# Performance work log

Measured on AMD Instinct MI355X. Metric: run time of the kernel, lower is better.

The kernel has to match this reference:

```python
import jax, jax.numpy as jnp
import numpy as np

S = 2048          # input sequence length
H_TOT = 4096      # total history tokens
NHIST = 1024      # number of history segments
LOC, TIM, UID = 50000, 48, 1000
D_LOC, D_TIM, D_UID, HID = 512, 64, 64, 512
D_IN = D_LOC + D_TIM          # 576, GRU input size
TARGET = 1024


def setup_inputs() -> dict:
    key = jax.random.key(0)
    ks = jax.random.split(key, 16)
    n = lambda k, shp, s=0.02: jax.random.normal(k, shp, dtype=jnp.float32) * s
    return {
        "loc": jax.random.randint(ks[0], (S, 1), 0, LOC),
        "tim": jax.random.randint(ks[1], (S, 1), 0, TIM),
        "history_loc": jax.random.randint(ks[2], (H_TOT, 1), 0, LOC),
        "history_tim": jax.random.randint(ks[3], (H_TOT, 1), 0, TIM),
        "history_count": jnp.full((NHIST,), H_TOT // NHIST, dtype=jnp.int32),
        "uid": jax.random.randint(ks[4], (1,), 0, UID),
        "target_len": TARGET,
        "emb_loc": n(ks[5], (LOC, D_LOC)),
        "emb_tim": n(ks[6], (TIM, D_TIM)),
        "emb_uid": n(ks[7], (UID, D_UID)),
        "fc_attn_w": n(ks[8], (HID, D_IN), 0.05),
        "fc_attn_b": jnp.zeros((HID,), jnp.float32),
        "w_ih": n(ks[9], (3 * HID, D_IN), 0.05),
        "w_hh": n(ks[10], (3 * HID, HID), 0.05),
        "b_ih": jnp.zeros((3 * HID,), jnp.float32),
        "b_hh": jnp.zeros((3 * HID,), jnp.float32),
        "fc_final_w": n(ks[11], (LOC, 2 * HID + D_UID), 0.05),
        "fc_final_b": jnp.zeros((LOC,), jnp.float32),
    }


def _gru(x, w_ih, w_hh, b_ih, b_hh):
    # x: [S, D_IN]; batch size 1 -> carry a single hidden vector. PyTorch GRU cell.
    gi = x @ w_ih.T + b_ih  # [S, 3H] (input projections precomputed)

    def step(h, gi_t):
        gh = w_hh @ h + b_hh
        i_r, i_z, i_n = jnp.split(gi_t, 3)
        h_r, h_z, h_n = jnp.split(gh, 3)
        r = jax.nn.sigmoid(i_r + h_r)
        z = jax.nn.sigmoid(i_z + h_z)
        nn_ = jnp.tanh(i_n + r * h_n)
        h_new = (1.0 - z) * nn_ + z * h
        return h_new, h_new

    _, out = jax.lax.scan(step, jnp.zeros((HID,), x.dtype), gi)
    return out  # [S, HID]


def reference(loc, tim, history_loc, history_tim, history_count, uid, target_len,
              emb_loc, emb_tim, emb_uid, fc_attn_w, fc_attn_b,
              w_ih, w_hh, b_ih, b_hh, fc_final_w, fc_final_b):
    # current trajectory embeddings (dropout is identity at eval)
    x = jnp.concatenate([emb_loc[loc[:, 0]], emb_tim[tim[:, 0]]], axis=1)  # [S, D_IN]

    # ragged segment-mean pooling of history loc embeddings, first-token tim embedding
    hist_le = emb_loc[history_loc[:, 0]]  # [H_TOT, D_LOC]
    hist_te = emb_tim[history_tim[:, 0]]  # [H_TOT, D_TIM]
    counts = history_count
    seg_ids = jnp.repeat(jnp.arange(NHIST), counts, total_repeat_length=H_TOT)
    loc2 = jax.ops.segment_sum(hist_le, seg_ids, num_segments=NHIST)
    loc2 = loc2 / counts[:, None].astype(loc2.dtype)
    offsets = jnp.cumsum(counts) - counts  # start index of each segment
    tim2 = hist_te[offsets]
    history = jnp.tanh(jnp.concatenate([loc2, tim2], axis=1) @ fc_attn_w.T + fc_attn_b)  # [NHIST, HID]

    out_state = _gru(x, w_ih, w_hh, b_ih, b_hh)  # [S, HID]
    q = out_state[-target_len:]                  # [T, HID]

    # dot attention: replaces the python double loop with one matmul + softmax
    attn = jax.nn.softmax(q @ history.T, axis=-1)  # [T, NHIST]
    context = attn @ history                       # [T, HID]

    uid_emb = jnp.broadcast_to(emb_uid[uid[0]], (target_len, D_UID))
    out = jnp.concatenate([q, context, uid_emb], axis=1)  # [T, 2H+D_UID]
    y = out @ fc_final_w.T + fc_final_b                   # [T, LOC]
    return jax.nn.log_softmax(y, axis=-1)
```

## Files before the change

### kernel.cpp

```cpp
#include <hip/hip_runtime.h>
#include <cstddef>

typedef unsigned short u16;
typedef unsigned int u32;

#define S_LEN   2048
#define H_TOT   4096
#define NHIST   1024
#define D_LOC   512
#define D_TIM   64
#define D_UID   64
#define HID     512
#define D_IN    576
#define TARGET  1024
#define NLOC    50000
#define D_OUT   1088
#define G3      1536

__device__ __forceinline__ u16 f2bf(float f) {
    u32 x; __builtin_memcpy(&x, &f, 4);
    u32 r = x + 0x7fffu + ((x >> 16) & 1u);
    return (u16)(r >> 16);
}
__device__ __forceinline__ float bf2f(u16 u) {
    u32 x = ((u32)u) << 16;
    float f; __builtin_memcpy(&f, &x, 4); return f;
}
__device__ __forceinline__ float u32_as_f32(u32 x) {
    float f; __builtin_memcpy(&f, &x, 4); return f;
}
__device__ __forceinline__ float sigm(float x) {
    return 1.0f / (1.0f + __expf(-x));
}
__device__ __forceinline__ float tanh_stable(float x) {
    float a = __expf(-2.0f * fabsf(x));
    float t = (1.0f - a) / (1.0f + a);
    return copysignf(t, x);
}
__device__ __forceinline__ u32 pk(float a, float b) {
    return (u32)f2bf(a) | ((u32)f2bf(b) << 16);
}

typedef __bf16 bf16x8 __attribute__((ext_vector_type(8)));
typedef float  f32x4  __attribute__((ext_vector_type(4)));

__global__ __launch_bounds__(1024) void scan_kernel(const int* __restrict__ counts,
                                                    int* __restrict__ offs) {
    __shared__ int s[NHIST];
    int tid = threadIdx.x;
    int v = counts[tid];
    s[tid] = v;
    __syncthreads();
    for (int d = 1; d < NHIST; d <<= 1) {
        int t = (tid >= d) ? s[tid - d] : 0;
        __syncthreads();
        s[tid] += t;
        __syncthreads();
    }
    offs[tid] = s[tid] - v;
}

__global__ __launch_bounds__(64) void hist_kernel(const int* __restrict__ hloc,
                                                  const int* __restrict__ htim,
                                                  const int* __restrict__ counts,
                                                  const int* __restrict__ offs,
                                                  const float* __restrict__ emb_loc,
                                                  const float* __restrict__ emb_tim,
                                                  u16* __restrict__ hist2) {
    int i = blockIdx.x, c = threadIdx.x;
    int off = offs[i], cnt = counts[i];
    float a[8] = {};
    for (int k = 0; k < cnt; k++) {
        int kk = off + k; if (kk >= H_TOT) break;
        const float* p = emb_loc + (size_t)hloc[kk] * D_LOC + c * 8;
        float4 q0 = ((const float4*)p)[0];
        float4 q1 = ((const float4*)p)[1];
        a[0] += q0.x; a[1] += q0.y; a[2] += q0.z; a[3] += q0.w;
        a[4] += q1.x; a[5] += q1.y; a[6] += q1.z; a[7] += q1.w;
    }
    float inv = (cnt > 0) ? 1.0f / (float)cnt : 0.0f;
    u16* o = hist2 + (size_t)i * D_IN + c * 8;
    #pragma unroll
    for (int j = 0; j < 8; j++) o[j] = f2bf(a[j] * inv);
    hist2[(size_t)i * D_IN + D_LOC + c] = f2bf(emb_tim[(size_t)htim[off] * D_TIM + c]);
}

__global__ __launch_bounds__(256) void build_x_kernel(const int* __restrict__ loc,
                                                      const int* __restrict__ tim,
                                                      const float* __restrict__ emb_loc,
                                                      const float* __restrict__ emb_tim,
                                                      u16* __restrict__ x) {
    int idx = blockIdx.x * 256 + threadIdx.x;
    int row = idx / D_IN, col = idx - row * D_IN;
    float v = (col < D_LOC) ? emb_loc[(size_t)loc[row] * D_LOC + col]
                            : emb_tim[(size_t)tim[row] * D_TIM + (col - D_LOC)];
    x[idx] = f2bf(v);
}

__global__ __launch_bounds__(256) void uid_kernel(const int* __restrict__ uid,
                                                  const float* __restrict__ emb_uid,
                                                  u16* __restrict__ outbuf) {
    int idx = blockIdx.x * 256 + threadIdx.x;
    int row = idx >> 6, c = idx & 63;
    outbuf[(size_t)row * D_OUT + 2 * HID + c] = f2bf(emb_uid[(size_t)uid[0] * D_UID + c]);
}

template<int EPI, bool OBF16, bool NG, bool AF32, bool BF32>
__global__ __launch_bounds__(256)
void gemm_bt_kernel(const void* __restrict__ Ap, const void* __restrict__ Bp,
                    void* __restrict__ Cp, const float* __restrict__ bias,
                    u16* __restrict__ Ct,
                    int M, int N, int K, int lda, int ldb, int ldc, int ldt) {
    __shared__ __align__(16) u16 sA[128 * 64];
    __shared__ __align__(16) u16 sB[128 * 64];
    const int tid = threadIdx.x;
    const int w = tid >> 6, lane = tid & 63;
    const int wr = (w >> 1) * 64, wc = (w & 1) * 64;
    const int m0 = blockIdx.y * 128, n0 = blockIdx.x * 128;
    f32x4 acc[4][4] = {};
    const int srow = w * 32 + (lane >> 3);
    const int scol = (lane & 7) * 8;

    for (int kt = 0; kt < K; kt += 64) {
        #pragma unroll
        for (int i = 0; i < 4; i++) {
            int rt = srow + i * 8;
            int ra = m0 + rt;
            if (AF32) {
                const float* s = (const float*)Ap + (size_t)ra * lda + kt + scol;
                float4 x0 = ((const float4*)s)[0];
                float4 x1 = ((const float4*)s)[1];
                uint4 q = { pk(x0.x, x0.y), pk(x0.z, x0.w), pk(x1.x, x1.y), pk(x1.z, x1.w) };
                *(uint4*)&sA[rt * 64 + scol] = q;
            } else {
                *(uint4*)&sA[rt * 64 + scol] =
                    *(const uint4*)((const u16*)Ap + (size_t)ra * lda + kt + scol);
            }
            int rb = n0 + rt;
            if (NG) rb = (rb < N - 1) ? rb : (N - 1);
            if (BF32) {
                const float* s = (const float*)Bp + (size_t)rb * ldb + kt + scol;
                float4 x0 = ((const float4*)s)[0];
                float4 x1 = ((const float4*)s)[1];
                uint4 q = { pk(x0.x, x0.y), pk(x0.z, x0.w), pk(x1.x, x1.y), pk(x1.z, x1.w) };
                *(uint4*)&sB[rt * 64 + scol] = q;
            } else {
                *(uint4*)&sB[rt * 64 + scol] =
                    *(const uint4*)((const u16*)Bp + (size_t)rb * ldb + kt + scol);
            }
        }
        __syncthreads();
        #pragma unroll
        for (int kk = 0; kk < 64; kk += 32) {
            const int krow = kk + (lane >> 4) * 8;
            bf16x8 af[4], bf_[4];
            #pragma unroll
            for (int mi = 0; mi < 4; mi++)
                af[mi] = *(const bf16x8*)&sA[(wr + mi * 16 + (lane & 15)) * 64 + krow];
            #pragma unroll
            for (int ni = 0; ni < 4; ni++)
                bf_[ni] = *(const bf16x8*)&sB[(wc + ni * 16 + (lane & 15)) * 64 + krow];
            #pragma unroll
            for (int mi = 0; mi < 4; mi++)
                #pragma unroll
                for (int ni = 0; ni < 4; ni++)
                    acc[mi][ni] = __builtin_amdgcn_mfma_f32_16x16x32_bf16(
                        af[mi], bf_[ni], acc[mi][ni], 0, 0, 0);
        }
        __syncthreads();
    }
    #pragma unroll
    for (int mi = 0; mi < 4; mi++) {
        #pragma unroll
        for (int ni = 0; ni < 4; ni++) {
            int gc = n0 + wc + ni * 16 + (lane & 15);
            if (NG && gc >= N) continue;
            #pragma unroll
            for (int r = 0; r < 4; r++) {
                int gr = m0 + wr + mi * 16 + (lane >> 4) * 4 + r;
                float v = acc[mi][ni][r];
                if (EPI & 1) v += bias[gc];
                if (EPI & 2) v = tanh_stable(v);
                if (OBF16) ((u16*)Cp)[(size_t)gr * ldc + gc] = f2bf(v);
                else       ((float*)Cp)[(size_t)gr * ldc + gc] = v;
                if (EPI & 4) Ct[(size_t)gc * ldt + gr] = f2bf(v);
            }
        }
    }
}

#define GRU_BLOCKS 16
__global__ __launch_bounds__(384, 2)
void gru_kernel(const float* __restrict__ gi, const float* __restrict__ w_hh,
                const float* __restrict__ b_hh, u32* __restrict__ hcomm,
                u16* __restrict__ outbuf) {
    const int b = blockIdx.x, tid = threadIdx.x;
    const int wr = tid % 96, qd = tid / 96;
    const int g = wr >> 5, jj = wr & 31;
    const int grow = g * HID + b * 32 + jj;

    __shared__ __align__(16) float hbuf[HID];
    __shared__ float psum[96 * 4];
    __shared__ float ghh[96], gii[96];

    float wreg[128];
    {
        const float4* wp = (const float4*)(w_hh + (size_t)grow * HID + qd * 128);
        #pragma unroll
        for (int c = 0; c < 32; c++) {
            float4 v = wp[c];
            wreg[c * 4 + 0] = v.x; wreg[c * 4 + 1] = v.y;
            wreg[c * 4 + 2] = v.z; wreg[c * 4 + 3] = v.w;
        }
    }
    float bhh = b_hh[grow];
    for (int i = tid; i < HID; i += 384) hbuf[i] = 0.0f;
    float gi_cur = (qd == 0) ? gi[grow] : 0.0f;
    __syncthreads();

    for (int t = 0; t < S_LEN; t++) {
        float acc = 0.0f;
        const float4* hp = (const float4*)(hbuf + qd * 128);
        #pragma unroll
        for (int c = 0; c < 32; c++) {
            float4 h4 = hp[c];
            acc = fmaf(wreg[4 * c + 0], h4.x, acc);
            acc = fmaf(wreg[4 * c + 1], h4.y, acc);
            acc = fmaf(wreg[4 * c + 2], h4.z, acc);
            acc = fmaf(wreg[4 * c + 3], h4.w, acc);
        }
        psum[wr * 4 + qd] = acc;
        __syncthreads();
        if (tid < 96) {
            float s = psum[tid * 4] + psum[tid * 4 + 1] + psum[tid * 4 + 2] + psum[tid * 4 + 3];
            ghh[tid] = s + bhh;
            gii[tid] = gi_cur;
        }
        __syncthreads();

        const u32 want = (u32)(t + 1);
        const int p = (t + 1) & 1;
        if (tid < 32) {
            float r = sigm(gii[tid] + ghh[tid]);
            float z = sigm(gii[32 + tid] + ghh[32 + tid]);
            float n = tanh_stable(gii[64 + tid] + r * ghh[64 + tid]);
            float hn = (1.0f - z) * n + z * hbuf[b * 32 + tid];
            u32 bits = (u32)f2bf(hn);
            __hip_atomic_store(&hcomm[p * HID + b * 32 + tid], (bits << 16) | want,
                               __ATOMIC_RELAXED, __HIP_MEMORY_SCOPE_AGENT);
            if (t >= (S_LEN - TARGET))
                outbuf[(size_t)(t - (S_LEN - TARGET)) * D_OUT + b * 32 + tid] = (u16)bits;
        }
        float gi_nxt = 0.0f;
        if (qd == 0) {
            int tn = (t + 1 < S_LEN) ? (t + 1) : (S_LEN - 1);
            gi_nxt = gi[(size_t)tn * G3 + grow];
        }
        if (t < S_LEN - 1) {
            u32 v;
            int w0 = tid;
            do {
                v = __hip_atomic_load(&hcomm[p * HID + w0], __ATOMIC_RELAXED, __HIP_MEMORY_SCOPE_AGENT);
            } while ((v & 0xffffu) != want);
            hbuf[w0] = u32_as_f32(v & 0xffff0000u);
            if (tid < 128) {
                int w1 = 384 + tid;
                do {
                    v = __hip_atomic_load(&hcomm[p * HID + w1], __ATOMIC_RELAXED, __HIP_MEMORY_SCOPE_AGENT);
                } while ((v & 0xffffu) != want);
                hbuf[w1] = u32_as_f32(v & 0xffff0000u);
            }
        }
        __syncthreads();
        gi_cur = gi_nxt;
    }
}

__global__ __launch_bounds__(256) void softmax_kernel(const float* __restrict__ sc,
                                                      u16* __restrict__ attn) {
    int r = blockIdx.x, tid = threadIdx.x;
    int lane = tid & 63, wv = tid >> 6;
    const float* row = sc + (size_t)r * NHIST;
    float v[4], m = -3.4e38f;
    #pragma unroll
    for (int k = 0; k < 4; k++) { v[k] = row[tid + 256 * k]; m = fmaxf(m, v[k]); }
    #pragma unroll
    for (int o = 32; o >= 1; o >>= 1) m = fmaxf(m, __shfl_xor(m, o));
    __shared__ float rmax[4], rsum[4];
    if (lane == 0) rmax[wv] = m;
    __syncthreads();
    m = fmaxf(fmaxf(rmax[0], rmax[1]), fmaxf(rmax[2], rmax[3]));
    float s = 0.0f;
    #pragma unroll
    for (int k = 0; k < 4; k++) { v[k] = __expf(v[k] - m); s += v[k]; }
    #pragma unroll
    for (int o = 32; o >= 1; o >>= 1) s += __shfl_xor(s, o);
    if (lane == 0) rsum[wv] = s;
    __syncthreads();
    s = rsum[0] + rsum[1] + rsum[2] + rsum[3];
    float inv = 1.0f / s;
    #pragma unroll
    for (int k = 0; k < 4; k++) attn[(size_t)r * NHIST + tid + 256 * k] = f2bf(v[k] * inv);
}

__global__ __launch_bounds__(1024) void logsoftmax_kernel(float* __restrict__ y) {
    int r = blockIdx.x, tid = threadIdx.x;
    int lane = tid & 63, wv = tid >> 6;
    float* row = y + (size_t)r * NLOC;
    __shared__ float red[16];
    float m = -3.4e38f;
    for (int i = tid; i < NLOC; i += 1024) m = fmaxf(m, row[i]);
    #pragma unroll
    for (int o = 32; o >= 1; o >>= 1) m = fmaxf(m, __shfl_xor(m, o));
    if (lane == 0) red[wv] = m;
    __syncthreads();
    #pragma unroll
    for (int k = 0; k < 16; k++) m = fmaxf(m, red[k]);
    __syncthreads();
    float s = 0.0f;
    for (int i = tid; i < NLOC; i += 1024) s += __expf(row[i] - m);
    #pragma unroll
    for (int o = 32; o >= 1; o >>= 1) s += __shfl_xor(s, o);
    if (lane == 0) red[wv] = s;
    __syncthreads();
    float tot = 0.0f;
    #pragma unroll
    for (int k = 0; k < 16; k++) tot += red[k];
    float lse = m + logf(tot);
    for (int i = tid; i < NLOC; i += 1024) row[i] = row[i] - lse;
}

extern "C" void kernel_launch(void* const* d_in, const int* in_sizes, int n_in,
                              void* d_out, int out_size, void* d_ws, size_t ws_size,
                              hipStream_t stream) {
    const int*   loc       = (const int*)d_in[0];
    const int*   tim       = (const int*)d_in[1];
    const int*   hloc      = (const int*)d_in[2];
    const int*   htim      = (const int*)d_in[3];
    const int*   counts    = (const int*)d_in[4];
    const int*   uid       = (const int*)d_in[5];
    const float* emb_loc   = (const float*)d_in[7];
    const float* emb_tim   = (const float*)d_in[8];
    const float* emb_uid   = (const float*)d_in[9];
    const float* fc_attn_w = (const float*)d_in[10];
    const float* fc_attn_b = (const float*)d_in[11];
    const float* w_ih      = (const float*)d_in[12];
    const float* w_hh      = (const float*)d_in[13];
    const float* b_ih      = (const float*)d_in[14];
    const float* b_hh      = (const float*)d_in[15];
    const float* fc_final_w= (const float*)d_in[16];
    const float* fc_final_b= (const float*)d_in[17];

    char* ws = (char*)d_ws;
    int*   offs     = (int*)(ws + 0);
    u32*   hcomm    = (u32*)(ws + 4096);
    u16*   hist2    = (u16*)(ws + 8192);
    u16*   xbuf     = (u16*)(ws + 1187840);
    u16*   history  = (u16*)(ws + 3547136);
    u16*   historyT = (u16*)(ws + 4595712);
    u16*   outbuf   = (u16*)(ws + 5644288);
    float* scores   = (float*)(ws + 7872512);
    u16*   attn     = (u16*)(ws + 12066816);
    float* gi       = (float*)(ws + 14163968);

    float* out = (float*)d_out;

    scan_kernel<<<1, 1024, 0, stream>>>(counts, offs);
    hist_kernel<<<NHIST, 64, 0, stream>>>(hloc, htim, counts, offs, emb_loc, emb_tim, hist2);
    build_x_kernel<<<(S_LEN * D_IN) / 256, 256, 0, stream>>>(loc, tim, emb_loc, emb_tim, xbuf);
    uid_kernel<<<(TARGET * D_UID) / 256, 256, 0, stream>>>(uid, emb_uid, outbuf);

    gemm_bt_kernel<1 | 2 | 4, true, false, false, true><<<dim3(HID / 128, NHIST / 128), 256, 0, stream>>>(
        hist2, fc_attn_w, history, fc_attn_b, historyT,
        NHIST, HID, D_IN, D_IN, D_IN, HID, NHIST);

    gemm_bt_kernel<1, false, false, false, true><<<dim3(G3 / 128, S_LEN / 128), 256, 0, stream>>>(
        xbuf, w_ih, gi, b_ih, nullptr,
        S_LEN, G3, D_IN, D_IN, D_IN, G3, 0);

    gru_kernel<<<GRU_BLOCKS, 384, 0, stream>>>(gi, w_hh, b_hh, hcomm, outbuf);

    gemm_bt_kernel<0, false, false, false, false><<<dim3(NHIST / 128, TARGET / 128), 256, 0, stream>>>(
        outbuf, history, scores, nullptr, nullptr,
        TARGET, NHIST, HID, D_OUT, HID, NHIST, 0);

    softmax_kernel<<<TARGET, 256, 0, stream>>>(scores, attn);

    gemm_bt_kernel<0, true, false, false, false><<<dim3(HID / 128, TARGET / 128), 256, 0, stream>>>(
        attn, historyT, outbuf + HID, nullptr, nullptr,
        TARGET, HID, NHIST, NHIST, NHIST, D_OUT, 0);

    gemm_bt_kernel<1, false, true, false, true><<<dim3((NLOC + 127) / 128, TARGET / 128), 256, 0, stream>>>(
        outbuf, fc_final_w, out, fc_final_b, nullptr,
        TARGET, NLOC, D_OUT, D_OUT, D_OUT, NLOC, 0);

    logsoftmax_kernel<<<TARGET, 1024, 0, stream>>>(out);
}
```

Baseline: 4.863 ms.

## Place all GRU blocks on one XCC and poll hidden state via L2-local loads

The GRU kernel now launches 128 blocks. Each block reads its XCC id and registers with a per-XCC counter. The first XCC to collect 16 blocks is elected, and only those 16 run the recurrence, so all cross-block hidden-state exchange stays within one XCC's shared L2. The spin loop also uses sc0 global loads for most polls and falls back to agent-scope atomics every 8th iteration, aiming to cut per-step synchronisation latency. The control words share workspace with the attn buffer, and the scheme risks deadlock if the 16 blocks of an XCC are never co-resident.

Measured after the change: 5.868 ms. +20.7%, slower.

```diff
diff --git a/kernel.cpp b/kernel.cpp
--- a/kernel.cpp
+++ b/kernel.cpp
@@ -40,14 +40,22 @@
 __device__ __forceinline__ u32 pk(float a, float b) {
     return (u32)f2bf(a) | ((u32)f2bf(b) << 16);
 }
+__device__ __forceinline__ u32 ld_sc0(const u32* p) {
+    u32 v;
+    asm volatile("global_load_dword %0, %1, off sc0\n\ts_waitcnt vmcnt(0)"
+                 : "=v"(v) : "v"(p));
+    return v;
+}
 
 typedef __bf16 bf16x8 __attribute__((ext_vector_type(8)));
 typedef float  f32x4  __attribute__((ext_vector_type(4)));
 
 __global__ __launch_bounds__(1024) void scan_kernel(const int* __restrict__ counts,
-                                                    int* __restrict__ offs) {
+                                                    int* __restrict__ offs,
+                                                    u32* __restrict__ ctrl) {
     __shared__ int s[NHIST];
     int tid = threadIdx.x;
+    if (tid < 16) ctrl[tid] = 0;
     int v = counts[tid];
     s[tid] = v;
     __syncthreads();
@@ -190,11 +198,34 @@
 }
 
 #define GRU_BLOCKS 16
+#define GRU_GRID   128
 __global__ __launch_bounds__(384, 2)
 void gru_kernel(const float* __restrict__ gi, const float* __restrict__ w_hh,
                 const float* __restrict__ b_hh, u32* __restrict__ hcomm,
-                u16* __restrict__ outbuf) {
-    const int b = blockIdx.x, tid = threadIdx.x;
+                u16* __restrict__ outbuf, u32* __restrict__ ctrl) {
+    __shared__ int s_b;
+    if (threadIdx.x == 0) {
+        u32 xcc;
+        asm volatile("s_getreg_b32 %0, hwreg(HW_REG_XCC_ID)" : "=s"(xcc));
+        xcc &= 7u;
+        u32 r = __hip_atomic_fetch_add(&ctrl[xcc], 1u,
+                                       __ATOMIC_RELAXED, __HIP_MEMORY_SCOPE_AGENT);
+        if (r == GRU_BLOCKS - 1) {
+            u32 expected = 0u;
+            __hip_atomic_compare_exchange_strong(&ctrl[8], &expected, xcc + 1u,
+                __ATOMIC_RELAXED, __ATOMIC_RELAXED, __HIP_MEMORY_SCOPE_AGENT);
+        }
+        u32 ch;
+        do {
+            ch = __hip_atomic_load(&ctrl[8], __ATOMIC_RELAXED, __HIP_MEMORY_SCOPE_AGENT);
+        } while (ch == 0u);
+        s_b = (r < GRU_BLOCKS && ch == xcc + 1u) ? (int)r : -1;
+    }
+    __syncthreads();
+    const int b = s_b;
+    if (b < 0) return;
+
+    const int tid = threadIdx.x;
     const int wr = tid % 96, qd = tid / 96;
     const int g = wr >> 5, jj = wr & 31;
     const int grow = g * HID + b * 32 + jj;
@@ -257,16 +288,26 @@
             gi_nxt = gi[(size_t)tn * G3 + grow];
         }
         if (t < S_LEN - 1) {
-            u32 v;
+            u32 v; int spin;
             int w0 = tid;
+            spin = 0;
             do {
-                v = __hip_atomic_load(&hcomm[p * HID + w0], __ATOMIC_RELAXED, __HIP_MEMORY_SCOPE_AGENT);
+                if ((++spin & 7) == 0)
+                    v = __hip_atomic_load(&hcomm[p * HID + w0], __ATOMIC_RELAXED,
+                                          __HIP_MEMORY_SCOPE_AGENT);
+                else
+                    v = ld_sc0(&hcomm[p * HID + w0]);
             } while ((v & 0xffffu) != want);
             hbuf[w0] = u32_as_f32(v & 0xffff0000u);
             if (tid < 128) {
                 int w1 = 384 + tid;
+                spin = 0;
                 do {
-                    v = __hip_atomic_load(&hcomm[p * HID + w1], __ATOMIC_RELAXED, __HIP_MEMORY_SCOPE_AGENT);
+                    if ((++spin & 7) == 0)
+                        v = __hip_atomic_load(&hcomm[p * HID + w1], __ATOMIC_RELAXED,
+                                              __HIP_MEMORY_SCOPE_AGENT);
+                    else
+                        v = ld_sc0(&hcomm[p * HID + w1]);
                 } while ((v & 0xffffu) != want);
                 hbuf[w1] = u32_as_f32(v & 0xffff0000u);
             }
@@ -362,10 +403,11 @@
     float* scores   = (float*)(ws + 7872512);
     u16*   attn     = (u16*)(ws + 12066816);
     float* gi       = (float*)(ws + 14163968);
+    u32*   ctrl     = (u32*)(ws + 12066816);
 
     float* out = (float*)d_out;
 
-    scan_kernel<<<1, 1024, 0, stream>>>(counts, offs);
+    scan_kernel<<<1, 1024, 0, stream>>>(counts, offs, ctrl);
     hist_kernel<<<NHIST, 64, 0, stream>>>(hloc, htim, counts, offs, emb_loc, emb_tim, hist2);
     build_x_kernel<<<(S_LEN * D_IN) / 256, 256, 0, stream>>>(loc, tim, emb_loc, emb_tim, xbuf);
     uid_kernel<<<(TARGET * D_UID) / 256, 256, 0, stream>>>(uid, emb_uid, outbuf);
@@ -378,7 +420,7 @@
         xbuf, w_ih, gi, b_ih, nullptr,
         S_LEN, G3, D_IN, D_IN, D_IN, G3, 0);
 
-    gru_kernel<<<GRU_BLOCKS, 384, 0, stream>>>(gi, w_hh, b_hh, hcomm, outbuf);
+    gru_kernel<<<GRU_GRID, 384, 0, stream>>>(gi, w_hh, b_hh, hcomm, outbuf, ctrl);
 
     gemm_bt_kernel<0, false, false, false, false><<<dim3(NHIST / 128, TARGET / 128), 256, 0, stream>>>(
         outbuf, history, scores, nullptr, nullptr,
```
